# Kernel tuning notes

Hardware: AMD Instinct MI355X
Metric: run time of the kernel (lower is better)

The kernel has to match this reference:

```python
import jax, jax.numpy as jnp
import numpy as np

K = 20          # neighbors
EPS = 1e-5      # batch-norm eps (torch default)


def setup_inputs() -> dict:
    key = jax.random.key(0)
    k1, k2 = jax.random.split(key, 2)
    B, C, N = 16, 3, 2048
    out_dims, in_dims = 64, 2 * C
    x = jax.random.normal(k1, (B, C, N), dtype=jnp.float32)
    # Conv2d 1x1 weight, kaiming-style init as in init_layer: std = sqrt(2/(1*1*out))
    W = jax.random.normal(k2, (out_dims, in_dims), dtype=jnp.float32) * np.float32(np.sqrt(2.0 / out_dims))
    bn_weight = jnp.ones((out_dims,), dtype=jnp.float32)
    bn_bias = jnp.zeros((out_dims,), dtype=jnp.float32)
    return {"x": x, "W": W, "bn_weight": bn_weight, "bn_bias": bn_bias}


def _get_graph_feature(x, k):
    # x: (B, C, N)
    xx = jnp.sum(x * x, axis=1)                       # (B, N) squared norms
    inner = jnp.einsum('bcn,bcm->bnm', x, x)          # (B, N, N)
    pd = -xx[:, :, None] + 2.0 * inner - xx[:, None, :]  # -||xi - xj||^2
    _, idx = jax.lax.top_k(pd, k)                     # (B, N, k) nearest neighbors
    xt = jnp.transpose(x, (0, 2, 1))                  # (B, N, C)
    # gather neighbor features per batch: (N, C)[ (N, k) ] -> (N, k, C)
    neigh = jax.vmap(lambda feats, ind: feats[ind])(xt, idx)   # (B, N, k, C)
    center = jnp.broadcast_to(xt[:, :, None, :], neigh.shape)  # (B, N, k, C)
    feat = jnp.concatenate([neigh - center, center], axis=-1)  # (B, N, k, 2C)
    return jnp.transpose(feat, (0, 3, 1, 2))          # (B, 2C, N, k)


def reference(x, W, bn_weight, bn_bias):
    feat = _get_graph_feature(x, K)                   # (B, 2C, N, k)
    y = jnp.einsum('oc,bcnk->bonk', W, feat)          # 1x1 conv, no bias
    # BatchNorm2d_fw: fresh running stats + training=True -> plain batch stats
    mean = jnp.mean(y, axis=(0, 2, 3), keepdims=True)
    var = jnp.var(y, axis=(0, 2, 3), keepdims=True)   # biased variance
    yn = (y - mean) * jax.lax.rsqrt(var + EPS)
    yn = yn * bn_weight[None, :, None, None] + bn_bias[None, :, None, None]
    out = jnp.max(jax.nn.relu(yn), axis=-1)           # max over k -> (B, 64, N)
    return out
```

## Files before the change

### kernel.cpp

```cpp
#include <hip/hip_runtime.h>
#include <math.h>

#define B_   16
#define N_   2048
#define KNN  20
#define OD   64
#define M_TOT (B_ * N_ * KNN)
#define PPB  64
#define NB   64
#define CAP  96
#define BKT_BASE 468

typedef unsigned long long u64;
typedef unsigned int u32;
typedef unsigned short u16;

__global__ __launch_bounds__(256) void k0_pack(const float* __restrict__ x,
                                               float4* __restrict__ g) {
    int i = blockIdx.x * 256 + threadIdx.x;
    int b = i >> 11, n = i & (N_ - 1);
    const float* xb = x + b * 3 * N_;
    float x0 = xb[n], x1 = xb[N_ + n], x2 = xb[2 * N_ + n];
    float xx = x0 * x0;
    xx = fmaf(x1, x1, xx);
    xx = fmaf(x2, x2, xx);
    g[i] = make_float4(x0, x1, x2, xx);
}

__global__ __launch_bounds__(512, 4) void k1_knn(const float4* __restrict__ g,
                                                 float* __restrict__ stats,
                                                 float4* __restrict__ evec) {
    __shared__ u32 hist[NB * PPB];
    __shared__ u16 coll[PPB][CAP];
    __shared__ u32 pcnt[PPB];
    __shared__ u32 edgev[PPB];

    const int b     = blockIdx.x >> 5;
    const int chunk = blockIdx.x & 31;
    const int t     = threadIdx.x;
    const float4* gb = g + (b << 11);

    const int lane = t & 63;
    const int il   = (chunk << 6) + lane;
    const float4 pi = gb[il];

    for (int i = t; i < NB * PPB; i += 512) hist[i] = 0;
    if (t < PPB) pcnt[t] = 0;
    __syncthreads();

    const int jw = __builtin_amdgcn_readfirstlane((t >> 6) << 8);

    for (int jj = 0; jj < 256; jj += 4) {
        float4 q[4];
#pragma unroll
        for (int u = 0; u < 4; ++u) q[u] = gb[jw + jj + u];
#pragma unroll
        for (int u = 0; u < 4; ++u) {
            float dot = pi.x * q[u].x;
            dot = fmaf(pi.y, q[u].y, dot);
            dot = fmaf(pi.z, q[u].z, dot);
            float pd = fmaf(2.f, dot, -pi.w) - q[u].w;
            u32 nk = __float_as_uint(pd) & 0x7FFFFFFFu;
            int bkt = min(max((int)(nk >> 21) - BKT_BASE, 0), 63);
            atomicAdd(&hist[(bkt << 6) + lane], 1u);
        }
    }
    __syncthreads();

    if (t < PPB) {
        int cum = 0, tau = 63;
        for (int k = 0; k < NB; ++k) {
            cum += (int)hist[(k << 6) + t];
            if (cum >= KNN) { tau = k; break; }
        }
        edgev[t] = (u32)(BKT_BASE + 1 + tau) << 21;
    }
    __syncthreads();

    {
        const u32 edge = edgev[lane];
        for (int jj = 0; jj < 256; jj += 4) {
            float4 q[4];
#pragma unroll
            for (int u = 0; u < 4; ++u) q[u] = gb[jw + jj + u];
#pragma unroll
            for (int u = 0; u < 4; ++u) {
                float dot = pi.x * q[u].x;
                dot = fmaf(pi.y, q[u].y, dot);
                dot = fmaf(pi.z, q[u].z, dot);
                float pd = fmaf(2.f, dot, -pi.w) - q[u].w;
                u32 nk = __float_as_uint(pd) & 0x7FFFFFFFu;
                if (nk < edge) {
                    u32 pos = atomicAdd(&pcnt[lane], 1u);
                    if (pos < CAP) coll[lane][pos] = (u16)(jw + jj + u);
                }
            }
        }
    }
    __syncthreads();

    if (t < PPB) {
        const int cnt = min((int)pcnt[t], CAP);
        u64 d[KNN];
#pragma unroll
        for (int q = 0; q < KNN; ++q) d[q] = 0ull;
        for (int e = 0; e < cnt; ++e) {
            int j = coll[t][e];
            float4 pj = gb[j];
            float dot = pi.x * pj.x;
            dot = fmaf(pi.y, pj.y, dot);
            dot = fmaf(pi.z, pj.z, dot);
            float pd = fmaf(2.f, dot, -pi.w) - pj.w;
            u32 uu = __float_as_uint(pd);
            u32 mono = ((int)uu < 0) ? ~uu : (uu | 0x80000000u);
            u64 v = ((u64)mono << 32) | (u32)(~j);
            if (v > d[KNN - 1]) {
#pragma unroll
                for (int q = 0; q < KNN; ++q) {
                    u64 hi = (v > d[q]) ? v : d[q];
                    u64 lo = (v > d[q]) ? d[q] : v;
                    d[q] = hi; v = lo;
                }
            }
        }

        float4* ep = evec + ((b * KNN) << 11) + il;
        float se0 = 0.f, se1 = 0.f, se2 = 0.f;
        float see[6] = {0.f, 0.f, 0.f, 0.f, 0.f, 0.f};
#pragma unroll
        for (int r = 0; r < KNN; ++r) {
            int j = (int)(~(u32)d[r]);
            float4 pj = gb[j];
            float e0 = pj.x - pi.x, e1 = pj.y - pi.y, e2 = pj.z - pi.z;
            ep[r << 11] = make_float4(e0, e1, e2, 0.f);
            se0 += e0; se1 += e1; se2 += e2;
            see[0] = fmaf(e0, e0, see[0]);
            see[1] = fmaf(e0, e1, see[1]);
            see[2] = fmaf(e0, e2, see[2]);
            see[3] = fmaf(e1, e1, see[3]);
            see[4] = fmaf(e1, e2, see[4]);
            see[5] = fmaf(e2, e2, see[5]);
        }
        float c0 = pi.x, c1 = pi.y, c2 = pi.z;
        float v[27];
        v[0] = se0; v[1] = se1; v[2] = se2;
        v[3] = 20.f * c0; v[4] = 20.f * c1; v[5] = 20.f * c2;
        v[6]  = see[0];
        v[7]  = see[1];
        v[8]  = see[2];
        v[9]  = se0 * c0;
        v[10] = se0 * c1;
        v[11] = se0 * c2;
        v[12] = see[3];
        v[13] = see[4];
        v[14] = se1 * c0;
        v[15] = se1 * c1;
        v[16] = se1 * c2;
        v[17] = see[5];
        v[18] = se2 * c0;
        v[19] = se2 * c1;
        v[20] = se2 * c2;
        v[21] = 20.f * c0 * c0;
        v[22] = 20.f * c0 * c1;
        v[23] = 20.f * c0 * c2;
        v[24] = 20.f * c1 * c1;
        v[25] = 20.f * c1 * c2;
        v[26] = 20.f * c2 * c2;

#pragma unroll
        for (int m = 0; m < 27; ++m) {
            float sm = v[m];
#pragma unroll
            for (int off = 32; off > 0; off >>= 1) sm += __shfl_xor(sm, off);
            if (t == 0) atomicAdd(stats + m, sm);
        }
    }
}

__global__ void k2_fin(const float* __restrict__ stats, const float* __restrict__ W,
                       const float* __restrict__ bnw, const float* __restrict__ bnb,
                       float* __restrict__ wp) {
    const int o = threadIdx.x;
    float m[6];
#pragma unroll
    for (int c = 0; c < 6; ++c) m[c] = stats[c];
    float S[6][6];
    int p = 6;
#pragma unroll
    for (int a = 0; a < 6; ++a)
#pragma unroll
        for (int bb = a; bb < 6; ++bb) { S[a][bb] = stats[p]; S[bb][a] = stats[p]; ++p; }
    float w[6];
#pragma unroll
    for (int c = 0; c < 6; ++c) w[c] = W[o * 6 + c];

    const float invM = 1.f / (float)M_TOT;
    float mean = 0.f;
#pragma unroll
    for (int c = 0; c < 6; ++c) mean += w[c] * m[c];
    mean *= invM;
    float ey2 = 0.f;
#pragma unroll
    for (int a = 0; a < 6; ++a)
#pragma unroll
        for (int bb = 0; bb < 6; ++bb) ey2 += w[a] * w[bb] * S[a][bb];
    ey2 *= invM;
    float var   = ey2 - mean * mean;
    float scale = bnw[o] * rsqrtf(var + 1e-5f);
    float shift = bnb[o] - mean * scale;
#pragma unroll
    for (int c = 0; c < 6; ++c) wp[o * 8 + c] = w[c] * scale;
    wp[o * 8 + 6] = shift;
    wp[o * 8 + 7] = 0.f;
}

__global__ __launch_bounds__(256) void k3_out(const float4* __restrict__ g,
                                              const float* __restrict__ wp,
                                              const float4* __restrict__ evec,
                                              float* __restrict__ out) {
    __shared__ float4 sev[PPB * KNN];
    __shared__ float  lwp[OD * 8];

    const int b     = blockIdx.x >> 5;
    const int chunk = blockIdx.x & 31;
    const int t     = threadIdx.x;
    const int n0    = chunk << 6;

    for (int q = t; q < OD * 8; q += 256) lwp[q] = wp[q];
    for (int i = t; i < PPB * KNN; i += 256) {
        int r = i >> 6, nn = i & 63;
        sev[i] = evec[((b * KNN + r) << 11) + n0 + nn];
    }
    __syncthreads();

    const int nl  = t & 63;
    const int sub = t >> 6;
    const int n   = n0 + nl;
    const float4 pi = g[(b << 11) + n];
    float* ob = out + (size_t)b * OD * N_ + n;

#pragma unroll
    for (int cb = 0; cb < 2; ++cb) {
        const int o0 = sub * 16 + cb * 8;
        float w0[8], w1[8], w2[8], bs[8], acc[8];
#pragma unroll
        for (int c = 0; c < 8; ++c) {
            const float* wo = &lwp[(o0 + c) * 8];
            w0[c] = wo[0]; w1[c] = wo[1]; w2[c] = wo[2];
            float base = wo[6];
            base = fmaf(wo[3], pi.x, base);
            base = fmaf(wo[4], pi.y, base);
            base = fmaf(wo[5], pi.z, base);
            bs[c] = base;
            acc[c] = 0.f;
        }
#pragma unroll
        for (int r = 0; r < KNN; ++r) {
            float4 e = sev[(r << 6) + nl];
#pragma unroll
            for (int c = 0; c < 8; ++c) {
                float y = bs[c];
                y = fmaf(w0[c], e.x, y);
                y = fmaf(w1[c], e.y, y);
                y = fmaf(w2[c], e.z, y);
                acc[c] = fmaxf(acc[c], y);
            }
        }
#pragma unroll
        for (int c = 0; c < 8; ++c) ob[(size_t)(o0 + c) << 11] = acc[c];
    }
}

extern "C" void kernel_launch(void* const* d_in, const int* in_sizes, int n_in,
                              void* d_out, int out_size, void* d_ws, size_t ws_size,
                              hipStream_t stream) {
    const float* x   = (const float*)d_in[0];
    const float* W   = (const float*)d_in[1];
    const float* bnw = (const float*)d_in[2];
    const float* bnb = (const float*)d_in[3];
    float* out = (float*)d_out;

    float*  stats = (float*)d_ws;
    float*  wp    = (float*)((char*)d_ws + 1024);
    float4* pts_g = (float4*)((char*)d_ws + 4096);
    float4* evec  = (float4*)((char*)d_ws + 4096 + 524288);

    hipMemsetAsync(d_ws, 0, 128, stream);
    k0_pack<<<dim3(128), dim3(256), 0, stream>>>(x, pts_g);
    k1_knn<<<dim3(512), dim3(512), 0, stream>>>(pts_g, stats, evec);
    k2_fin<<<dim3(1), dim3(64), 0, stream>>>(stats, W, bnw, bnb, wp);
    k3_out<<<dim3(512), dim3(256), 0, stream>>>(pts_g, wp, evec, out);
}
```

Before: 250.9 us.

## Replace LDS atomic histogram with register threshold counts and two-pass refinement

The kNN threshold search used to build a 64-bucket LDS histogram with one atomicAdd per candidate pair. It now keeps per-thread register counters against 8 coarse exponent edges, then runs a second pass with 7 finer edges. Partial counts are packed into 16-bit halves in shared memory and reduced across waves. This removes LDS atomic contention at the cost of an extra full distance pass and more compares per pair. The candidate threshold may also end up tighter or looser than before, which changes how often collection hits CAP.

```diff
diff --git a/kernel.cpp b/kernel.cpp
--- a/kernel.cpp
+++ b/kernel.cpp
@@ -7,9 +7,8 @@
 #define OD   64
 #define M_TOT (B_ * N_ * KNN)
 #define PPB  64
-#define NB   64
 #define CAP  96
-#define BKT_BASE 468
+#define EDG(k) ((u32)(121 + 2 * (k)) << 23)
 
 typedef unsigned long long u64;
 typedef unsigned int u32;
@@ -30,10 +29,11 @@
 __global__ __launch_bounds__(512, 4) void k1_knn(const float4* __restrict__ g,
                                                  float* __restrict__ stats,
                                                  float4* __restrict__ evec) {
-    __shared__ u32 hist[NB * PPB];
+    __shared__ u32 cntb[4][8][PPB];
     __shared__ u16 coll[PPB][CAP];
     __shared__ u32 pcnt[PPB];
     __shared__ u32 edgev[PPB];
+    __shared__ u32 tauv[PPB];
 
     const int b     = blockIdx.x >> 5;
     const int chunk = blockIdx.x & 31;
@@ -41,56 +41,113 @@
     const float4* gb = g + (b << 11);
 
     const int lane = t & 63;
+    const int w    = t >> 6;
     const int il   = (chunk << 6) + lane;
     const float4 pi = gb[il];
 
-    for (int i = t; i < NB * PPB; i += 512) hist[i] = 0;
-    if (t < PPB) pcnt[t] = 0;
-    __syncthreads();
-
-    const int jw = __builtin_amdgcn_readfirstlane((t >> 6) << 8);
-
-    for (int jj = 0; jj < 256; jj += 4) {
-        float4 q[4];
-#pragma unroll
-        for (int u = 0; u < 4; ++u) q[u] = gb[jw + jj + u];
-#pragma unroll
-        for (int u = 0; u < 4; ++u) {
+    const int jw = w << 8;
+    int jv;
+    asm volatile("v_mov_b32 %0, %1" : "=v"(jv) : "s"(jw));
+
+    u32 cnt[8] = {0, 0, 0, 0, 0, 0, 0, 0};
+    for (int jj = 0; jj < 256; jj += 8) {
+        float4 q[8];
+#pragma unroll
+        for (int u = 0; u < 8; ++u) q[u] = gb[jv + jj + u];
+#pragma unroll
+        for (int u = 0; u < 8; ++u) {
             float dot = pi.x * q[u].x;
             dot = fmaf(pi.y, q[u].y, dot);
             dot = fmaf(pi.z, q[u].z, dot);
             float pd = fmaf(2.f, dot, -pi.w) - q[u].w;
             u32 nk = __float_as_uint(pd) & 0x7FFFFFFFu;
-            int bkt = min(max((int)(nk >> 21) - BKT_BASE, 0), 63);
-            atomicAdd(&hist[(bkt << 6) + lane], 1u);
-        }
-    }
+#pragma unroll
+            for (int k = 0; k < 8; ++k) cnt[k] += (nk < EDG(k)) ? 1u : 0u;
+        }
+    }
+#pragma unroll
+    for (int k2 = 0; k2 < 4; ++k2)
+        cntb[k2][w][lane] = cnt[2 * k2] | (cnt[2 * k2 + 1] << 16);
     __syncthreads();
 
     if (t < PPB) {
-        int cum = 0, tau = 63;
-        for (int k = 0; k < NB; ++k) {
-            cum += (int)hist[(k << 6) + t];
-            if (cum >= KNN) { tau = k; break; }
-        }
-        edgev[t] = (u32)(BKT_BASE + 1 + tau) << 21;
+        u32 tot[8] = {0, 0, 0, 0, 0, 0, 0, 0};
+        for (int ww = 0; ww < 8; ++ww) {
+#pragma unroll
+            for (int k2 = 0; k2 < 4; ++k2) {
+                u32 v = cntb[k2][ww][t];
+                tot[2 * k2]     += v & 0xFFFFu;
+                tot[2 * k2 + 1] += v >> 16;
+            }
+        }
+        int ks = 7;
+#pragma unroll
+        for (int k = 6; k >= 0; --k) if (tot[k] >= KNN) ks = k;
+        edgev[t] = EDG(ks);
+        pcnt[t]  = 0;
+    }
+    __syncthreads();
+
+    const u32 eup = edgev[lane];
+    u32 qe[7];
+#pragma unroll
+    for (int k = 0; k < 7; ++k) qe[k] = eup - (2u << 23) + ((u32)(k + 1) << 21);
+    u32 qc[7] = {0, 0, 0, 0, 0, 0, 0};
+    for (int jj = 0; jj < 256; jj += 8) {
+        float4 q[8];
+#pragma unroll
+        for (int u = 0; u < 8; ++u) q[u] = gb[jv + jj + u];
+#pragma unroll
+        for (int u = 0; u < 8; ++u) {
+            float dot = pi.x * q[u].x;
+            dot = fmaf(pi.y, q[u].y, dot);
+            dot = fmaf(pi.z, q[u].z, dot);
+            float pd = fmaf(2.f, dot, -pi.w) - q[u].w;
+            u32 nk = __float_as_uint(pd) & 0x7FFFFFFFu;
+#pragma unroll
+            for (int k = 0; k < 7; ++k) qc[k] += (nk < qe[k]) ? 1u : 0u;
+        }
+    }
+#pragma unroll
+    for (int k2 = 0; k2 < 3; ++k2)
+        cntb[k2][w][lane] = qc[2 * k2] | (qc[2 * k2 + 1] << 16);
+    cntb[3][w][lane] = qc[6];
+    __syncthreads();
+
+    if (t < PPB) {
+        u32 qt[7] = {0, 0, 0, 0, 0, 0, 0};
+        for (int ww = 0; ww < 8; ++ww) {
+#pragma unroll
+            for (int k2 = 0; k2 < 3; ++k2) {
+                u32 v = cntb[k2][ww][t];
+                qt[2 * k2]     += v & 0xFFFFu;
+                qt[2 * k2 + 1] += v >> 16;
+            }
+            qt[6] += cntb[3][ww][t];
+        }
+        u32 eu = edgev[t];
+        u32 tau = eu;
+#pragma unroll
+        for (int k = 6; k >= 0; --k)
+            if (qt[k] >= KNN) tau = eu - (2u << 23) + ((u32)(k + 1) << 21);
+        tauv[t] = tau;
     }
     __syncthreads();
 
     {
-        const u32 edge = edgev[lane];
-        for (int jj = 0; jj < 256; jj += 4) {
-            float4 q[4];
-#pragma unroll
-            for (int u = 0; u < 4; ++u) q[u] = gb[jw + jj + u];
-#pragma unroll
-            for (int u = 0; u < 4; ++u) {
+        const u32 tau = tauv[lane];
+        for (int jj = 0; jj < 256; jj += 8) {
+            float4 q[8];
+#pragma unroll
+            for (int u = 0; u < 8; ++u) q[u] = gb[jv + jj + u];
+#pragma unroll
+            for (int u = 0; u < 8; ++u) {
                 float dot = pi.x * q[u].x;
                 dot = fmaf(pi.y, q[u].y, dot);
                 dot = fmaf(pi.z, q[u].z, dot);
                 float pd = fmaf(2.f, dot, -pi.w) - q[u].w;
                 u32 nk = __float_as_uint(pd) & 0x7FFFFFFFu;
-                if (nk < edge) {
+                if (nk < tau) {
                     u32 pos = atomicAdd(&pcnt[lane], 1u);
                     if (pos < CAP) coll[lane][pos] = (u16)(jw + jj + u);
                 }
@@ -100,11 +157,11 @@
     __syncthreads();
 
     if (t < PPB) {
-        const int cnt = min((int)pcnt[t], CAP);
+        const int cnt2 = min((int)pcnt[t], CAP);
         u64 d[KNN];
 #pragma unroll
         for (int q = 0; q < KNN; ++q) d[q] = 0ull;
-        for (int e = 0; e < cnt; ++e) {
+        for (int e = 0; e < cnt2; ++e) {
             int j = coll[t][e];
             float4 pj = gb[j];
             float dot = pi.x * pj.x;
```

After: 289.8 us. 15.5% more time.

## Replace shared-memory atomic histogram with register threshold counts in KNN kernel

Applied to the files above, without the earlier changes.

The first KNN pass previously built a 64-bucket histogram with LDS atomics for every candidate. It now counts candidates against 14 power-of-two distance thresholds in registers and reduces those counts across 16 waves through packed shared-memory words. Blocks grow to 1024 threads so each wave scans 128 candidates, and the collection pass splits candidates into four sub-buckets so the top-k insertion sort only visits the sub-buckets it needs. This removes atomic contention in the first pass, but the coarser thresholds may admit more candidates and hit the collection cap more often. It also adds register pressure under the 1024-thread launch bound.

```diff
diff --git a/kernel.cpp b/kernel.cpp
--- a/kernel.cpp
+++ b/kernel.cpp
@@ -7,9 +7,7 @@
 #define OD   64
 #define M_TOT (B_ * N_ * KNN)
 #define PPB  64
-#define NB   64
 #define CAP  96
-#define BKT_BASE 468
 
 typedef unsigned long long u64;
 typedef unsigned int u32;
@@ -27,13 +25,13 @@
     g[i] = make_float4(x0, x1, x2, xx);
 }
 
-__global__ __launch_bounds__(512, 4) void k1_knn(const float4* __restrict__ g,
-                                                 float* __restrict__ stats,
-                                                 float4* __restrict__ evec) {
-    __shared__ u32 hist[NB * PPB];
-    __shared__ u16 coll[PPB][CAP];
-    __shared__ u32 pcnt[PPB];
-    __shared__ u32 edgev[PPB];
+__global__ __launch_bounds__(1024, 8) void k1_knn(const float4* __restrict__ g,
+                                                  float* __restrict__ stats,
+                                                  float4* __restrict__ evec) {
+    __shared__ u32 cntb[7][16][PPB];
+    __shared__ u16 coll[4 * CAP * PPB];
+    __shared__ u32 pcnt[4][PPB];
+    __shared__ u32 topv[PPB];
 
     const int b     = blockIdx.x >> 5;
     const int chunk = blockIdx.x & 31;
@@ -41,58 +39,81 @@
     const float4* gb = g + (b << 11);
 
     const int lane = t & 63;
-    const int il   = (chunk << 6) + lane;
+    const int il0  = chunk << 6;
+    const int il   = il0 + lane;
     const float4 pi = gb[il];
 
-    for (int i = t; i < NB * PPB; i += 512) hist[i] = 0;
-    if (t < PPB) pcnt[t] = 0;
+    if (t < 256) pcnt[t >> 6][t & 63] = 0;
+
+    const int jw = __builtin_amdgcn_readfirstlane((t >> 6) << 7);
+    int jv;
+    asm volatile("v_mov_b32 %0, %1" : "=v"(jv) : "s"(jw));
+
+    const float negedge[14] = {
+        -0.00390625f, -0.0078125f, -0.015625f, -0.03125f, -0.0625f, -0.125f,
+        -0.25f, -0.5f, -1.f, -2.f, -4.f, -8.f, -16.f, -32.f};
+    u32 cnt[14] = {0,0,0,0,0,0,0,0,0,0,0,0,0,0};
+    for (int jj = 0; jj < 128; jj += 4) {
+        float4 c4[4];
+#pragma unroll
+        for (int u = 0; u < 4; ++u) c4[u] = gb[jv + jj + u];
+#pragma unroll
+        for (int u = 0; u < 4; ++u) {
+            float dot = pi.x * c4[u].x;
+            dot = fmaf(pi.y, c4[u].y, dot);
+            dot = fmaf(pi.z, c4[u].z, dot);
+            float pd = fmaf(2.f, dot, -pi.w) - c4[u].w;
+#pragma unroll
+            for (int k = 0; k < 14; ++k) cnt[k] += (pd > negedge[k]) ? 1u : 0u;
+        }
+    }
+    {
+        const int w = t >> 6;
+#pragma unroll
+        for (int p = 0; p < 7; ++p)
+            cntb[p][w][lane] = cnt[2 * p] | (cnt[2 * p + 1] << 16);
+    }
     __syncthreads();
 
-    const int jw = __builtin_amdgcn_readfirstlane((t >> 6) << 8);
-
-    for (int jj = 0; jj < 256; jj += 4) {
-        float4 q[4];
-#pragma unroll
-        for (int u = 0; u < 4; ++u) q[u] = gb[jw + jj + u];
-#pragma unroll
-        for (int u = 0; u < 4; ++u) {
-            float dot = pi.x * q[u].x;
-            dot = fmaf(pi.y, q[u].y, dot);
-            dot = fmaf(pi.z, q[u].z, dot);
-            float pd = fmaf(2.f, dot, -pi.w) - q[u].w;
-            u32 nk = __float_as_uint(pd) & 0x7FFFFFFFu;
-            int bkt = min(max((int)(nk >> 21) - BKT_BASE, 0), 63);
-            atomicAdd(&hist[(bkt << 6) + lane], 1u);
-        }
+    if (t < PPB) {
+        u32 tot[14] = {0,0,0,0,0,0,0,0,0,0,0,0,0,0};
+        for (int ww = 0; ww < 16; ++ww) {
+#pragma unroll
+            for (int p = 0; p < 7; ++p) {
+                u32 v = cntb[p][ww][t];
+                tot[2 * p]     += v & 0xFFFFu;
+                tot[2 * p + 1] += v >> 16;
+            }
+        }
+        int ks = 13;
+#pragma unroll
+        for (int k = 12; k >= 0; --k) if (tot[k] >= KNN) ks = k;
+        topv[t] = (u32)(119 + ks) << 23;
     }
     __syncthreads();
 
-    if (t < PPB) {
-        int cum = 0, tau = 63;
-        for (int k = 0; k < NB; ++k) {
-            cum += (int)hist[(k << 6) + t];
-            if (cum >= KNN) { tau = k; break; }
-        }
-        edgev[t] = (u32)(BKT_BASE + 1 + tau) << 21;
-    }
-    __syncthreads();
-
     {
-        const u32 edge = edgev[lane];
-        for (int jj = 0; jj < 256; jj += 4) {
-            float4 q[4];
-#pragma unroll
-            for (int u = 0; u < 4; ++u) q[u] = gb[jw + jj + u];
+        const u32 T  = topv[lane];
+        const u32 s1 = T - 0x600000u;
+        const u32 s2 = T - 0x400000u;
+        const u32 s3 = T - 0x200000u;
+        for (int jj = 0; jj < 128; jj += 4) {
+            float4 c4[4];
+#pragma unroll
+            for (int u = 0; u < 4; ++u) c4[u] = gb[jv + jj + u];
 #pragma unroll
             for (int u = 0; u < 4; ++u) {
-                float dot = pi.x * q[u].x;
-                dot = fmaf(pi.y, q[u].y, dot);
-                dot = fmaf(pi.z, q[u].z, dot);
-                float pd = fmaf(2.f, dot, -pi.w) - q[u].w;
+                float dot = pi.x * c4[u].x;
+                dot = fmaf(pi.y, c4[u].y, dot);
+                dot = fmaf(pi.z, c4[u].z, dot);
+                float pd = fmaf(2.f, dot, -pi.w) - c4[u].w;
                 u32 nk = __float_as_uint(pd) & 0x7FFFFFFFu;
-                if (nk < edge) {
-                    u32 pos = atomicAdd(&pcnt[lane], 1u);
-                    if (pos < CAP) coll[lane][pos] = (u16)(jw + jj + u);
+                u32 qq = ((nk >= s1) ? 1u : 0u) + ((nk >= s2) ? 1u : 0u) +
+                         ((nk >= s3) ? 1u : 0u);
+                if (nk < T) {
+                    u32 pos = atomicAdd(&pcnt[qq][lane], 1u);
+                    if (pos < CAP)
+                        coll[((qq * CAP + pos) << 6) + lane] = (u16)(jw + jj + u);
                 }
             }
         }
@@ -100,26 +121,35 @@
     __syncthreads();
 
     if (t < PPB) {
-        const int cnt = min((int)pcnt[t], CAP);
+        u32 c0 = pcnt[0][t], c1 = pcnt[1][t], c2 = pcnt[2][t], c3 = pcnt[3][t];
+        (void)c3;
+        int qs; u32 cum = c0;
+        if (cum >= KNN) qs = 0;
+        else { cum += c1; if (cum >= KNN) qs = 1;
+               else { cum += c2; qs = (cum >= KNN) ? 2 : 3; } }
+
         u64 d[KNN];
 #pragma unroll
         for (int q = 0; q < KNN; ++q) d[q] = 0ull;
-        for (int e = 0; e < cnt; ++e) {
-            int j = coll[t][e];
-            float4 pj = gb[j];
-            float dot = pi.x * pj.x;
-            dot = fmaf(pi.y, pj.y, dot);
-            dot = fmaf(pi.z, pj.z, dot);
-            float pd = fmaf(2.f, dot, -pi.w) - pj.w;
-            u32 uu = __float_as_uint(pd);
-            u32 mono = ((int)uu < 0) ? ~uu : (uu | 0x80000000u);
-            u64 v = ((u64)mono << 32) | (u32)(~j);
-            if (v > d[KNN - 1]) {
-#pragma unroll
-                for (int q = 0; q < KNN; ++q) {
-                    u64 hi = (v > d[q]) ? v : d[q];
-                    u64 lo = (v > d[q]) ? d[q] : v;
-                    d[q] = hi; v = lo;
+        for (int qq = 0; qq <= qs; ++qq) {
+            const int cc = min((int)pcnt[qq][t], CAP);
+            for (int e = 0; e < cc; ++e) {
+                int j = coll[((qq * CAP + e) << 6) + t];
+                float4 pj = gb[j];
+                float dot = pi.x * pj.x;
+                dot = fmaf(pi.y, pj.y, dot);
+                dot = fmaf(pi.z, pj.z, dot);
+                float pd = fmaf(2.f, dot, -pi.w) - pj.w;
+                u32 uu = __float_as_uint(pd);
+                u32 mono = ((int)uu < 0) ? ~uu : (uu | 0x80000000u);
+                u64 v = ((u64)mono << 32) | (u32)(~j);
+                if (v > d[KNN - 1]) {
+#pragma unroll
+                    for (int q = 0; q < KNN; ++q) {
+                        u64 hi = (v > d[q]) ? v : d[q];
+                        u64 lo = (v > d[q]) ? d[q] : v;
+                        d[q] = hi; v = lo;
+                    }
                 }
             }
         }
@@ -141,31 +171,31 @@
             see[4] = fmaf(e1, e2, see[4]);
             see[5] = fmaf(e2, e2, see[5]);
         }
-        float c0 = pi.x, c1 = pi.y, c2 = pi.z;
+        float cx = pi.x, cy = pi.y, cz = pi.z;
         float v[27];
         v[0] = se0; v[1] = se1; v[2] = se2;
-        v[3] = 20.f * c0; v[4] = 20.f * c1; v[5] = 20.f * c2;
+        v[3] = 20.f * cx; v[4] = 20.f * cy; v[5] = 20.f * cz;
         v[6]  = see[0];
         v[7]  = see[1];
         v[8]  = see[2];
-        v[9]  = se0 * c0;
-        v[10] = se0 * c1;
-        v[11] = se0 * c2;
+        v[9]  = se0 * cx;
+        v[10] = se0 * cy;
+        v[11] = se0 * cz;
         v[12] = see[3];
         v[13] = see[4];
-        v[14] = se1 * c0;
-        v[15] = se1 * c1;
-        v[16] = se1 * c2;
+        v[14] = se1 * cx;
+        v[15] = se1 * cy;
+        v[16] = se1 * cz;
         v[17] = see[5];
-        v[18] = se2 * c0;
-        v[19] = se2 * c1;
-        v[20] = se2 * c2;
-        v[21] = 20.f * c0 * c0;
-        v[22] = 20.f * c0 * c1;
-        v[23] = 20.f * c0 * c2;
-        v[24] = 20.f * c1 * c1;
-        v[25] = 20.f * c1 * c2;
-        v[26] = 20.f * c2 * c2;
+        v[18] = se2 * cx;
+        v[19] = se2 * cy;
+        v[20] = se2 * cz;
+        v[21] = 20.f * cx * cx;
+        v[22] = 20.f * cx * cy;
+        v[23] = 20.f * cx * cz;
+        v[24] = 20.f * cy * cy;
+        v[25] = 20.f * cy * cz;
+        v[26] = 20.f * cz * cz;
 
 #pragma unroll
         for (int m = 0; m < 27; ++m) {
@@ -287,7 +317,7 @@
 
     hipMemsetAsync(d_ws, 0, 128, stream);
     k0_pack<<<dim3(128), dim3(256), 0, stream>>>(x, pts_g);
-    k1_knn<<<dim3(512), dim3(512), 0, stream>>>(pts_g, stats, evec);
+    k1_knn<<<dim3(512), dim3(1024), 0, stream>>>(pts_g, stats, evec);
     k2_fin<<<dim3(1), dim3(64), 0, stream>>>(stats, W, bnw, bnb, wp);
     k3_out<<<dim3(512), dim3(256), 0, stream>>>(pts_g, wp, evec, out);
 }
```

New measurement: 398.4 us. 1.59x slower.
